# Optimization experiments

Measured on AMD Instinct MI355X. Metric: run time of the kernel, lower is better.

Reference implementation:

```python
import jax, jax.numpy as jnp
import numpy as np

EPS = 1e-5
POOL = 4  # two stacked AvgPool3d(2) == one AvgPool3d(4, stride=4) on the valid region


def setup_inputs() -> dict:
    key = jax.random.key(0)
    k1, k2, k3 = jax.random.split(key, 3)
    N, Cin, Cout, D = 16, 32, 16, 32
    x = jax.random.normal(k1, (N, Cin, D, D, D), dtype=jnp.float32)
    w = jax.random.normal(k2, (Cin, Cout, 3, 3, 3), dtype=jnp.float32) * 0.1
    b = jax.random.normal(k3, (Cout,), dtype=jnp.float32) * 0.1
    gamma = jnp.ones((Cout,), dtype=jnp.float32)
    beta = jnp.zeros((Cout,), dtype=jnp.float32)
    return {"x": x, "w": w, "b": b, "gamma": gamma, "beta": beta}


def _convT_bn_pool(x, w, b, gamma, beta):
    # ConvTranspose3d(stride=2, padding=1, K=3) == dilated conv with
    # lhs_dilation=2, padding=K-1-p=1, spatially-flipped kernel, IO->OI swap.
    wt = jnp.flip(w, axis=(2, 3, 4)).transpose(1, 0, 2, 3, 4)  # [Cout,Cin,3,3,3]
    y = jax.lax.conv_general_dilated(
        x, wt,
        window_strides=(1, 1, 1),
        padding=[(1, 1), (1, 1), (1, 1)],
        lhs_dilation=(2, 2, 2),
        dimension_numbers=("NCDHW", "OIDHW", "NCDHW"),
    )
    y = y + b[None, :, None, None, None]  # [N,Cout,Dout,Hout,Wout], Dout=2D-1

    # BatchNorm training stats: biased variance over (N,D,H,W) per channel
    mean = jnp.mean(y, axis=(0, 2, 3, 4), keepdims=True)
    var = jnp.mean(jnp.square(y - mean), axis=(0, 2, 3, 4), keepdims=True)
    inv = jax.lax.rsqrt(var + EPS)
    yn = (y - mean) * inv * gamma[None, :, None, None, None] + beta[None, :, None, None, None]

    # Two AvgPool3d(2) == AvgPool3d(4, stride 4) on the cropped valid region
    N_, C_, Do, Ho, Wo = yn.shape
    D2, H2, W2 = Do // POOL, Ho // POOL, Wo // POOL
    yn = yn[:, :, : D2 * POOL, : H2 * POOL, : W2 * POOL]
    yn = yn.reshape(N_, C_, D2, POOL, H2, POOL, W2, POOL)
    return jnp.mean(yn, axis=(3, 5, 7))  # [N,C,D2,H2,W2]


def reference(x, w, b, gamma, beta):
    return _convT_bn_pool(x, w, b, gamma, beta)
```

## Files before the change

kernel.cpp:

```cpp
#include <hip/hip_runtime.h>


typedef __attribute__((ext_vector_type(8))) short bf16x8;
typedef __attribute__((ext_vector_type(4))) float f32x4;

static __device__ __forceinline__ unsigned short f2bf(float f) {
    unsigned int u = __float_as_uint(f);
    u = (u + 0x7fffu + ((u >> 16) & 1u)) >> 16;
    return (unsigned short)u;
}
static __device__ __forceinline__ unsigned cvtpk(float a, float b) {
    unsigned r;
    asm("v_cvt_pk_bf16_f32 %0, %1, %2" : "=v"(r) : "v"(a), "v"(b));
    return r;
}

__global__ __launch_bounds__(256)
void kw(const float* __restrict__ w, unsigned short* __restrict__ wT)
{
    const int idx = blockIdx.x * 256 + threadIdx.x;
    if (idx < 13824) {
        const int ci = idx & 31, co = (idx >> 5) & 15, tap = idx >> 9;
        wT[idx] = f2bf(w[(ci * 16 + co) * 27 + tap]);
    }
}

__global__ __launch_bounds__(256, 2)
void convf2(const float* __restrict__ x,
            const unsigned short* __restrict__ wT,
            const float* __restrict__ bias,
            float* __restrict__ pooled,
            float* __restrict__ psum, float* __restrict__ psq)
{
    const int ht = blockIdx.x, dt = blockIdx.y, bz = blockIdx.z;
    const int n0 = bz * 4;
    const int tid = threadIdx.x;
    const int v = tid >> 6, lane = tid & 63;
    const int tw = v & 1, odp = v >> 1;
    const int c = lane & 15, qd = lane >> 4;

    __shared__ alignas(16) unsigned short xs[2][9504];
    __shared__ alignas(16) unsigned short wTs[13824];
    __shared__ float sred[4][16], qred[4][16], pbuf[2][2][8][16];

    const float bv = bias[c];

    #pragma unroll
    for (int i = 0; i < 7; ++i) {
        const int chunk = v + 4 * i;
        if (chunk < 27) {
            __builtin_amdgcn_global_load_lds(
                (const char*)wT + chunk * 1024 + lane * 16,
                (char*)wTs + chunk * 1024,
                16, 0, 0);
        }
    }

    const int ciS = tid >> 3, q = tid & 7;
    const int oL = ciS & 7;
    int  offp[9]; bool okp[9];
    #pragma unroll
    for (int p = 0; p < 9; ++p) {
        const int di = p / 3, hi = p - 3*(p/3);
        const int id = 2*dt + di, ih = 2*ht + hi;
        okp[p]  = (id < 32) && (ih < 32);
        offp[p] = id*1024 + ih*32;
    }
    float4 F[9];
    auto ISSUE = [&](int nn) {
        const float* xb = x + (size_t)(nn*32 + ciS)*32768 + 4*q;
        #pragma unroll
        for (int p = 0; p < 9; ++p)
            F[p] = okp[p] ? *(const float4*)(xb + offp[p])
                          : make_float4(0.f, 0.f, 0.f, 0.f);
    };
    const unsigned selP = (lane & 8) ? 0x07060302u : 0x01000504u;
    const int iwT = 4*q + (oL & 3), hT = oL >> 2;
    auto TRANSP = [&](int buf) {
        unsigned short* xp = &xs[buf][0];
        #pragma unroll
        for (int p = 0; p < 9; ++p) {
            unsigned u0 = cvtpk(F[p].x, F[p].y);
            unsigned u1 = cvtpk(F[p].z, F[p].w);
            const unsigned a0 = (unsigned)__shfl_xor((int)u0, 8, 64);
            const unsigned a1 = (unsigned)__shfl_xor((int)u1, 8, 64);
            u0 = __builtin_amdgcn_perm(u0, a0, selP);
            u1 = __builtin_amdgcn_perm(u1, a1, selP);
            const unsigned b0 = (unsigned)__shfl_xor((int)u0, 16, 64);
            const unsigned b1 = (unsigned)__shfl_xor((int)u1, 16, 64);
            const unsigned w0 = (lane & 16) ? b1 : u0;
            const unsigned w1 = (lane & 16) ? u1 : b0;
            *(uint2*)(xp + p*1056 + v*264 + iwT*8 + 4*hT) = make_uint2(w0, w1);
        }
    };

    ISSUE(n0);
    if (tid < 36) {
        const int dihi = tid >> 2, gg = tid & 3;
        *(uint4*)(&xs[0][0] + dihi*1056 + gg*264 + 256) = make_uint4(0,0,0,0);
        *(uint4*)(&xs[1][0] + dihi*1056 + gg*264 + 256) = make_uint4(0,0,0,0);
    }
    TRANSP(0);
    __syncthreads();

    constexpr int KHP[3][2][2] = {
        {{1,1},{2,3}},
        {{0,0},{1,2}},
        {{0,1},{1,3}},
    };
    const int PB[3]  = {9, 18, 0};
    const int POL[3] = {0, 1, 1};
    const int PDI[3] = {odp, odp, odp + 1};
    const int iwb = 16 * tw + c;
    auto LDB = [&](int tap) -> bf16x8 {
        return *(const bf16x8*)(wTs + tap*512 + c*32 + qd*8);
    };
    const bool pok = (dt < 15) && (ht < 15);

    float sA = 0.f, sqA = 0.f;
    float Pd[2] = {0.f, 0.f};

    auto POOLW = [&](int t) {
        if (odp == 1 && pok) {
            #pragma unroll
            for (int jj = 0; jj < 2; ++jj) {
                const int jl = 2*qd + jj, jg = 8*tw + jl;
                if (jg < 15) {
                    const float tot = pbuf[t & 1][tw][jl][c] + Pd[jj];
                    pooled[((n0 + t)*16 + c)*3375 + dt*225 + ht*15 + jg]
                        = tot * (1.f/64.f);
                }
            }
        }
    };

    for (int tt = 0; tt < 4; ++tt) {
        const int cur = tt & 1;
        if (tt < 3) ISSUE(n0 + tt + 1);
        if (tt > 0) POOLW(tt - 1);

        const unsigned short* xcur = &xs[cur][0];
        auto LDA = [&](int dihi, int sofs) -> bf16x8 {
            return *(const bf16x8*)(xcur + dihi*1056 + qd*264 + (iwb + sofs)*8);
        };

        f32x4 acc[2][4][2];
        #pragma unroll
        for (int ol = 0; ol < 2; ++ol)
            #pragma unroll
            for (int oh = 0; oh < 4; ++oh)
                #pragma unroll
                for (int par = 0; par < 2; ++par)
                    acc[ol][oh][par] = (f32x4){0.f,0.f,0.f,0.f};

        bf16x8 B0 = LDB(9 + 0), B1 = LDB(9 + 1), B2 = LDB(9 + 2);
        #pragma unroll
        for (int s = 0; s < 9; ++s) {
            const int ph = s / 3;
            bf16x8 N0, N1, N2;
            if (s < 8) {
                const int sn = s + 1;
                const int phn = sn / 3, khn = sn - 3*(sn/3);
                const int bn_ = PB[phn] + khn * 3;
                N0 = LDB(bn_ + 0); N1 = LDB(bn_ + 1); N2 = LDB(bn_ + 2);
            }
            const int kh = s - 3*(s/3);
            const int ol = POL[ph], di = PDI[ph];
            #pragma unroll
            for (int pp = 0; pp < 2; ++pp) {
                const int hi = KHP[kh][pp][0], oh = KHP[kh][pp][1];
                const bf16x8 A0 = LDA(di*3 + hi, 0), A1 = LDA(di*3 + hi, 1);
                acc[ol][oh][0] = __builtin_amdgcn_mfma_f32_16x16x32_bf16(
                    A0, B1, acc[ol][oh][0], 0, 0, 0);
                acc[ol][oh][1] = __builtin_amdgcn_mfma_f32_16x16x32_bf16(
                    A1, B0, acc[ol][oh][1], 0, 0, 0);
                acc[ol][oh][1] = __builtin_amdgcn_mfma_f32_16x16x32_bf16(
                    A0, B2, acc[ol][oh][1], 0, 0, 0);
            }
            if (s < 8) { B0 = N0; B1 = N1; B2 = N2; }
        }

        float P[2] = {0.f, 0.f};
        #pragma unroll
        for (int ol = 0; ol < 2; ++ol) {
            const int odg = 2*odp + ol;
            const bool odok = !(dt == 15 && odg == 3);
            #pragma unroll
            for (int oh = 0; oh < 4; ++oh) {
                const bool ohok = !(ht == 15 && oh == 3);
                #pragma unroll
                for (int par = 0; par < 2; ++par)
                    #pragma unroll
                    for (int r = 0; r < 4; ++r) {
                        const float val = acc[ol][oh][par][r] + bv;
                        const bool owok = !(par == 1 && tw == 1 && qd == 3 && r == 3);
                        const float mk = (odok && ohok && owok) ? 1.f : 0.f;
                        sA += mk * val; sqA += mk * val * val;
                        P[r >> 1] += val;
                    }
            }
        }
        if (odp == 0 && pok) {
            pbuf[cur][tw][2*qd + 0][c] = P[0];
            pbuf[cur][tw][2*qd + 1][c] = P[1];
        } else {
            Pd[0] = P[0]; Pd[1] = P[1];
        }

        if (tt < 3) TRANSP(cur ^ 1);
        __syncthreads();
    }

    POOLW(3);

    sA  += __shfl_xor(sA, 16, 64);  sA  += __shfl_xor(sA, 32, 64);
    sqA += __shfl_xor(sqA, 16, 64); sqA += __shfl_xor(sqA, 32, 64);
    if (lane < 16) { sred[v][lane] = sA; qred[v][lane] = sqA; }
    __syncthreads();
    if (tid < 16) {
        const int blk = (bz*16 + dt)*16 + ht;
        psum[tid*4096 + blk] = sred[0][tid]+sred[1][tid]+sred[2][tid]+sred[3][tid];
        psq [tid*4096 + blk] = qred[0][tid]+qred[1][tid]+qred[2][tid]+qred[3][tid];
    }
}

__global__ void bnfinal(const float* __restrict__ psum, const float* __restrict__ psq,
                        const float* __restrict__ gamma, const float* __restrict__ beta,
                        float* __restrict__ bn)
{
    const int co = blockIdx.x;
    const int t  = threadIdx.x;
    float S = 0, Q = 0;
    for (int blk = t; blk < 1024; blk += 256) {
        S += psum[co*4096 + blk];
        Q += psq [co*4096 + blk];
    }
    #pragma unroll
    for (int off = 32; off > 0; off >>= 1) {
        S += __shfl_down(S, off, 64);
        Q += __shfl_down(Q, off, 64);
    }
    __shared__ float rs[4], rq[4];
    if ((t & 63) == 0) { rs[t >> 6] = S; rq[t >> 6] = Q; }
    __syncthreads();
    if (t == 0) {
        S = rs[0] + rs[1] + rs[2] + rs[3];
        Q = rq[0] + rq[1] + rq[2] + rq[3];
        const float cnt = 16.f * 63.f * 63.f * 63.f;
        const float mean = S / cnt;
        const float var  = Q / cnt - mean * mean;
        const float inv  = rsqrtf(var + 1e-5f);
        const float sc   = inv * gamma[co];
        bn[co]      = sc;
        bn[16 + co] = beta[co] - mean * sc;
    }
}

__global__ void finalize(const float* __restrict__ pooled, const float* __restrict__ bn,
                         float* __restrict__ out)
{
    const int i  = blockIdx.x * 256 + threadIdx.x;
    const int co = (i / 3375) & 15;
    out[i] = pooled[i] * bn[co] + bn[16 + co];
}

extern "C" void kernel_launch(void* const* d_in, const int* in_sizes, int n_in,
                              void* d_out, int out_size, void* d_ws, size_t ws_size,
                              hipStream_t stream)
{
    const float* x     = (const float*)d_in[0];
    const float* w     = (const float*)d_in[1];
    const float* b     = (const float*)d_in[2];
    const float* gamma = (const float*)d_in[3];
    const float* beta  = (const float*)d_in[4];
    float* out = (float*)d_out;

    char* wsb = (char*)d_ws;
    unsigned short* wT = (unsigned short*)wsb;
    float* pooled = (float*)(wsb + 27648);
    float* psum   = (float*)(wsb + 27648 + 3456000);
    float* psq    = (float*)(wsb + 27648 + 3456000 + 262144);
    float* bn     = (float*)(wsb + 27648 + 3456000 + 2*262144);

    kw<<<54, 256, 0, stream>>>(w, wT);
    dim3 grid(16, 16, 4);
    convf2<<<grid, 256, 0, stream>>>(x, wT, b, pooled, psum, psq);
    bnfinal<<<16, 256, 0, stream>>>(psum, psq, gamma, beta, bn);
    finalize<<<3375, 256, 0, stream>>>(pooled, bn, out);
}
```

Measured before the change: 128.3 us.

## Single-buffer the input LDS tile to fit three blocks per CU

Drops the double-buffered x tile and the double-buffered pooling buffer in shared memory, cutting LDS use so three blocks can share a CU, and raises the launch-bounds occupancy hint to match. The transpose into LDS now happens after an extra barrier rather than overlapping with the MFMA loop of the previous batch element, and the pooled writes happen right after each iteration. This trades intra-block overlap for more resident blocks, adds a second __syncthreads per iteration, and tightens the register budget.

```diff
diff --git a/kernel.cpp b/kernel.cpp
--- a/kernel.cpp
+++ b/kernel.cpp
@@ -25,7 +25,7 @@
     }
 }
 
-__global__ __launch_bounds__(256, 2)
+__global__ __launch_bounds__(256, 3)
 void convf2(const float* __restrict__ x,
             const unsigned short* __restrict__ wT,
             const float* __restrict__ bias,
@@ -39,9 +39,9 @@
     const int tw = v & 1, odp = v >> 1;
     const int c = lane & 15, qd = lane >> 4;
 
-    __shared__ alignas(16) unsigned short xs[2][9504];
+    __shared__ alignas(16) unsigned short xs[9504];
     __shared__ alignas(16) unsigned short wTs[13824];
-    __shared__ float sred[4][16], qred[4][16], pbuf[2][2][8][16];
+    __shared__ float sred[4][16], qred[4][16], pbuf[2][8][16];
 
     const float bv = bias[c];
 
@@ -76,8 +76,7 @@
     };
     const unsigned selP = (lane & 8) ? 0x07060302u : 0x01000504u;
     const int iwT = 4*q + (oL & 3), hT = oL >> 2;
-    auto TRANSP = [&](int buf) {
-        unsigned short* xp = &xs[buf][0];
+    auto TRANSP = [&]() {
         #pragma unroll
         for (int p = 0; p < 9; ++p) {
             unsigned u0 = cvtpk(F[p].x, F[p].y);
@@ -90,17 +89,16 @@
             const unsigned b1 = (unsigned)__shfl_xor((int)u1, 16, 64);
             const unsigned w0 = (lane & 16) ? b1 : u0;
             const unsigned w1 = (lane & 16) ? u1 : b0;
-            *(uint2*)(xp + p*1056 + v*264 + iwT*8 + 4*hT) = make_uint2(w0, w1);
+            *(uint2*)(xs + p*1056 + v*264 + iwT*8 + 4*hT) = make_uint2(w0, w1);
         }
     };
 
     ISSUE(n0);
     if (tid < 36) {
         const int dihi = tid >> 2, gg = tid & 3;
-        *(uint4*)(&xs[0][0] + dihi*1056 + gg*264 + 256) = make_uint4(0,0,0,0);
-        *(uint4*)(&xs[1][0] + dihi*1056 + gg*264 + 256) = make_uint4(0,0,0,0);
-    }
-    TRANSP(0);
+        *(uint4*)(xs + dihi*1056 + gg*264 + 256) = make_uint4(0,0,0,0);
+    }
+    TRANSP();
     __syncthreads();
 
     constexpr int KHP[3][2][2] = {
@@ -115,34 +113,15 @@
     auto LDB = [&](int tap) -> bf16x8 {
         return *(const bf16x8*)(wTs + tap*512 + c*32 + qd*8);
     };
+    auto LDA = [&](int dihi, int sofs) -> bf16x8 {
+        return *(const bf16x8*)(xs + dihi*1056 + qd*264 + (iwb + sofs)*8);
+    };
     const bool pok = (dt < 15) && (ht < 15);
 
     float sA = 0.f, sqA = 0.f;
-    float Pd[2] = {0.f, 0.f};
-
-    auto POOLW = [&](int t) {
-        if (odp == 1 && pok) {
-            #pragma unroll
-            for (int jj = 0; jj < 2; ++jj) {
-                const int jl = 2*qd + jj, jg = 8*tw + jl;
-                if (jg < 15) {
-                    const float tot = pbuf[t & 1][tw][jl][c] + Pd[jj];
-                    pooled[((n0 + t)*16 + c)*3375 + dt*225 + ht*15 + jg]
-                        = tot * (1.f/64.f);
-                }
-            }
-        }
-    };
 
     for (int tt = 0; tt < 4; ++tt) {
-        const int cur = tt & 1;
         if (tt < 3) ISSUE(n0 + tt + 1);
-        if (tt > 0) POOLW(tt - 1);
-
-        const unsigned short* xcur = &xs[cur][0];
-        auto LDA = [&](int dihi, int sofs) -> bf16x8 {
-            return *(const bf16x8*)(xcur + dihi*1056 + qd*264 + (iwb + sofs)*8);
-        };
 
         f32x4 acc[2][4][2];
         #pragma unroll
@@ -201,17 +180,28 @@
             }
         }
         if (odp == 0 && pok) {
-            pbuf[cur][tw][2*qd + 0][c] = P[0];
-            pbuf[cur][tw][2*qd + 1][c] = P[1];
-        } else {
-            Pd[0] = P[0]; Pd[1] = P[1];
-        }
-
-        if (tt < 3) TRANSP(cur ^ 1);
+            pbuf[tw][2*qd + 0][c] = P[0];
+            pbuf[tw][2*qd + 1][c] = P[1];
+        }
+
         __syncthreads();
-    }
-
-    POOLW(3);
+
+        if (odp == 1 && pok) {
+            #pragma unroll
+            for (int jj = 0; jj < 2; ++jj) {
+                const int jl = 2*qd + jj, jg = 8*tw + jl;
+                if (jg < 15) {
+                    const float tot = pbuf[tw][jl][c] + P[jj];
+                    pooled[((n0 + tt)*16 + c)*3375 + dt*225 + ht*15 + jg]
+                        = tot * (1.f/64.f);
+                }
+            }
+        }
+        if (tt < 3) {
+            TRANSP();
+            __syncthreads();
+        }
+    }
 
     sA  += __shfl_xor(sA, 16, 64);  sA  += __shfl_xor(sA, 32, 64);
     sqA += __shfl_xor(sqA, 16, 64); sqA += __shfl_xor(sqA, 32, 64);
```

Result: slower. 135.5 us (+5.6%).
